# Kernel tuning notes

Measured on AMD Instinct MI355X. Metric: run time of the kernel, lower is better.

## Reference

```python
import jax, jax.numpy as jnp
import numpy as np

N_NODES = 50000
N_EDGES = 400000
N_GRAPHS = 500
N_FEAT = 4
EMB = 200
HID = 128


def setup_inputs() -> dict:
    key = jax.random.key(0)
    ks = jax.random.split(key, 16)
    x = jax.random.normal(ks[0], (N_NODES, N_FEAT), dtype=jnp.float32)
    edge_index = jax.random.randint(ks[1], (2, N_EDGES), 0, N_NODES, dtype=jnp.int64)
    x_scalar = jax.random.normal(ks[2], (N_GRAPHS, N_FEAT), dtype=jnp.float32)
    batch_index = jnp.sort(jax.random.randint(ks[3], (N_NODES,), 0, N_GRAPHS, dtype=jnp.int64))

    def lin(k, fan_in, fan_out):
        return jax.random.normal(k, (fan_in, fan_out), dtype=jnp.float32) / np.sqrt(fan_in)

    params = {
        'W0': lin(ks[4], N_FEAT, EMB), 'b0': jnp.zeros((EMB,), jnp.float32),
        'W1': lin(ks[5], EMB, EMB), 'b1': jnp.zeros((EMB,), jnp.float32),
        'W2': lin(ks[6], EMB, EMB), 'b2': jnp.zeros((EMB,), jnp.float32),
        'W3': lin(ks[7], EMB, EMB), 'b3': jnp.zeros((EMB,), jnp.float32),
        'Wl1': lin(ks[8], EMB + N_FEAT, HID),
        'bl1': jax.random.normal(ks[9], (HID,), jnp.float32) * 0.01,
        'Wl2': lin(ks[10], HID, 1),
        'bl2': jax.random.normal(ks[11], (1,), jnp.float32) * 0.01,
    }
    return dict(x=x, edge_index=edge_index, x_scalar=x_scalar, batch_index=batch_index, **params)


def _gcn_conv(h, W, b, src, dst, norm, num_nodes):
    # PyG GCNConv: h' = D^-1/2 (A+I) D^-1/2 (h W) + b, with precomputed edge norms
    m = (h @ W)[src] * norm[:, None]            # [E+N, out]
    out = jax.ops.segment_sum(m, dst, num_segments=num_nodes)
    return out + b


def reference(x, edge_index, x_scalar, batch_index,
              W0, b0, W1, b1, W2, b2, W3, b3, Wl1, bl1, Wl2, bl2):
    num_nodes = x.shape[0]
    loops = jnp.arange(num_nodes, dtype=edge_index.dtype)
    src = jnp.concatenate([edge_index[0], loops])  # self-loops appended
    dst = jnp.concatenate([edge_index[1], loops])
    deg = jax.ops.segment_sum(jnp.ones_like(dst, dtype=x.dtype), dst, num_segments=num_nodes)
    dinv = deg ** -0.5                              # deg >= 1 due to self-loops
    norm = dinv[src] * dinv[dst]

    h = jax.nn.leaky_relu(_gcn_conv(x, W0, b0, src, dst, norm, num_nodes), 0.01)
    h = jax.nn.leaky_relu(_gcn_conv(h, W1, b1, src, dst, norm, num_nodes), 0.01)
    h = jax.nn.leaky_relu(_gcn_conv(h, W2, b2, src, dst, norm, num_nodes), 0.01)
    h = jax.nn.leaky_relu(_gcn_conv(h, W3, b3, src, dst, norm, num_nodes), 0.01)

    # global mean pool per graph
    sums = jax.ops.segment_sum(h, batch_index, num_segments=N_GRAPHS)
    cnt = jax.ops.segment_sum(jnp.ones((num_nodes,), h.dtype), batch_index, num_segments=N_GRAPHS)
    pooled = sums / jnp.maximum(cnt, 1.0)[:, None]

    g = jnp.concatenate([pooled, x_scalar], axis=1)   # [G, EMB+4]
    g = jax.nn.leaky_relu(g @ Wl1 + bl1, 0.01)
    out = g @ Wl2 + bl2                                # [G, 1]
    return out
```

## Files before the change

kernel.cpp:

```cpp
#include <hip/hip_runtime.h>
#include <math.h>

#define LEAKY(v) ((v) > 0.0f ? (v) : 0.01f * (v))

typedef _Float16 v8h __attribute__((ext_vector_type(8)));
typedef float v4f __attribute__((ext_vector_type(4)));

__global__ void k_count(const int* __restrict__ ei, int* __restrict__ cnt, int E) {
    int e = blockIdx.x * blockDim.x + threadIdx.x;
    if (e < E) atomicAdd(&cnt[ei[E + e]], 1);
}

__global__ __launch_bounds__(256) void k_scan1(const int* __restrict__ cnt,
                                               int* __restrict__ rowptr,
                                               int* __restrict__ bsum, int n) {
    __shared__ int s[256];
    int t = threadIdx.x, i = blockIdx.x * 256 + t;
    int v = (i < n) ? cnt[i] : 0;
    s[t] = v;
    __syncthreads();
    for (int off = 1; off < 256; off <<= 1) {
        int u = (t >= off) ? s[t - off] : 0;
        __syncthreads();
        s[t] += u;
        __syncthreads();
    }
    if (i < n) rowptr[i] = s[t] - v;
    if (t == 255) bsum[blockIdx.x] = s[255];
}

__global__ __launch_bounds__(256) void k_scan3(int* __restrict__ rowptr,
                                               const int* __restrict__ bsum,
                                               const int* __restrict__ cnt,
                                               float* __restrict__ dinv, int n) {
    __shared__ int sred[256];
    int t = threadIdx.x;
    int accum = 0;
    for (int b = t; b < (int)blockIdx.x; b += 256) accum += bsum[b];
    sred[t] = accum;
    __syncthreads();
    for (int off = 128; off > 0; off >>= 1) {
        if (t < off) sred[t] += sred[t + off];
        __syncthreads();
    }
    int base = sred[0];
    int i = blockIdx.x * 256 + t;
    if (i < n) {
        rowptr[i] += base;
        dinv[i] = rsqrtf(1.0f + (float)cnt[i]);
    }
}

__global__ void k_fill(const int* __restrict__ ei, const float* __restrict__ dinv,
                       int* __restrict__ rowptr, int2* __restrict__ adj, int E) {
    int e = blockIdx.x * blockDim.x + threadIdx.x;
    if (e < E) {
        int s = ei[e], d = ei[E + e];
        int pos = atomicAdd(&rowptr[d], 1);
        adj[pos] = make_int2(s, __float_as_int(dinv[s] * dinv[d]));
    }
}

__global__ __launch_bounds__(256) void k_splitW3(const float* __restrict__ W1,
                                                 const float* __restrict__ W2,
                                                 const float* __restrict__ W3,
                                                 _Float16* __restrict__ th0, _Float16* __restrict__ tl0,
                                                 _Float16* __restrict__ th1, _Float16* __restrict__ tl1,
                                                 _Float16* __restrict__ th2, _Float16* __restrict__ tl2,
                                                 int* __restrict__ cnt, int n) {
    int layer = blockIdx.y;
    const float* W = (layer == 0) ? W1 : (layer == 1) ? W2 : W3;
    _Float16* Wth = (layer == 0) ? th0 : (layer == 1) ? th1 : th2;
    _Float16* Wtl = (layer == 0) ? tl0 : (layer == 1) ? tl1 : tl2;
    int idx = blockIdx.x * blockDim.x + threadIdx.x;
    int gidx = (blockIdx.y * gridDim.x + blockIdx.x) * 256 + threadIdx.x;
    for (int j = gidx; j < n; j += gridDim.x * gridDim.y * 256) cnt[j] = 0;
    if (idx >= 224 * 208) return;
    int k = idx / 208, c = idx - k * 208;
    float v = (k < 200 && c < 200) ? W[k * 200 + c] : 0.0f;
    _Float16 hi = (_Float16)v;
    _Float16 lo = (_Float16)(v - (float)hi);
    Wth[c * 224 + k] = hi;
    Wtl[c * 224 + k] = lo;
}

__global__ __launch_bounds__(512, 4) void k_gemm200_mfma_l0(const float* __restrict__ x,
                                                            const float* __restrict__ dinv,
                                                            const int* __restrict__ rowptr,
                                                            const int2* __restrict__ adj,
                                                            const float* __restrict__ W0,
                                                            const float* __restrict__ b0,
                                                            const _Float16* __restrict__ Wth,
                                                            const _Float16* __restrict__ Wtl,
                                                            _Float16* __restrict__ T, int M) {
    __shared__ _Float16 Wsh[2][208 * 32];
    __shared__ _Float16 Wsl[2][208 * 32];
    __shared__ float W0s[4][200];
    __shared__ float b0s[200];
    const int tid  = threadIdx.x;
    const int lane = tid & 63;
    const int wid  = tid >> 6;
    const int quad = lane >> 4;
    const int l16  = lane & 15;
    const int rowA = blockIdx.x * 128 + wid * 16 + l16;
    const int rowAc = min(rowA, M - 1);

    const int nr0 = tid >> 2, p0 = tid & 3;
    const bool two = (tid < 320);
    const int nr1 = nr0 + 128;
    uint4 rh0, rl0, rh1, rl1;
    rh0 = *(const uint4*)&Wth[nr0 * 224 + p0 * 8];
    rl0 = *(const uint4*)&Wtl[nr0 * 224 + p0 * 8];
    if (two) {
        rh1 = *(const uint4*)&Wth[nr1 * 224 + p0 * 8];
        rl1 = *(const uint4*)&Wtl[nr1 * 224 + p0 * 8];
    }

    for (int idx = tid; idx < 1000; idx += 512) {
        if (idx < 800) W0s[idx / 200][idx % 200] = W0[idx];
        else b0s[idx - 800] = b0[idx - 800];
    }

    float w0n = dinv[rowAc]; w0n *= w0n;
    float4 xv = ((const float4*)x)[rowAc];
    float4 pxv = make_float4(xv.x * w0n, xv.y * w0n, xv.z * w0n, xv.w * w0n);
    {
        int lo = rowAc ? rowptr[rowAc - 1] : 0;
        int hi = rowptr[rowAc];
        for (int j = lo; j < hi; ++j) {
            int2 cw = adj[j];
            float w = __int_as_float(cw.y);
            float4 sv = ((const float4*)x)[cw.x];
            pxv.x += sv.x * w; pxv.y += sv.y * w; pxv.z += sv.z * w; pxv.w += sv.w * w;
        }
    }

    v4f acc[13];
#pragma unroll
    for (int t = 0; t < 13; ++t) acc[t] = 0.0f;

#pragma unroll
    for (int kc = 0; kc < 7; ++kc) {
        const int k0 = kc * 32;
        const int buf = kc & 1;
        *(uint4*)&Wsh[buf][nr0 * 32 + p0 * 8] = rh0;
        *(uint4*)&Wsl[buf][nr0 * 32 + p0 * 8] = rl0;
        if (two) {
            *(uint4*)&Wsh[buf][nr1 * 32 + p0 * 8] = rh1;
            *(uint4*)&Wsl[buf][nr1 * 32 + p0 * 8] = rl1;
        }
        if (kc < 6) {
            rh0 = *(const uint4*)&Wth[nr0 * 224 + (k0 + 32) + p0 * 8];
            rl0 = *(const uint4*)&Wtl[nr0 * 224 + (k0 + 32) + p0 * 8];
            if (two) {
                rh1 = *(const uint4*)&Wth[nr1 * 224 + (k0 + 32) + p0 * 8];
                rl1 = *(const uint4*)&Wtl[nr1 * 224 + (k0 + 32) + p0 * 8];
            }
        }
        __syncthreads();
        v8h ah, al;
        int kb = k0 + quad * 8;
        if (kb < 200) {
#pragma unroll
            for (int j = 0; j < 8; ++j) {
                int k = kb + j;
                float pv = pxv.x * W0s[0][k] + pxv.y * W0s[1][k]
                         + pxv.z * W0s[2][k] + pxv.w * W0s[3][k] + b0s[k];
                pv = LEAKY(pv);
                _Float16 h = (_Float16)pv;
                ah[j] = h;
                al[j] = (_Float16)(pv - (float)h);
            }
        } else {
#pragma unroll
            for (int j = 0; j < 8; ++j) { ah[j] = (_Float16)0.0f; al[j] = (_Float16)0.0f; }
        }
#pragma unroll
        for (int t = 0; t < 13; ++t) {
            int nidx = (t * 16 + l16) * 32 + quad * 8;
            v8h wh = *(const v8h*)&Wsh[buf][nidx];
            v8h wl = *(const v8h*)&Wsl[buf][nidx];
            acc[t] = __builtin_amdgcn_mfma_f32_16x16x32_f16(ah, wh, acc[t], 0, 0, 0);
            acc[t] = __builtin_amdgcn_mfma_f32_16x16x32_f16(ah, wl, acc[t], 0, 0, 0);
            acc[t] = __builtin_amdgcn_mfma_f32_16x16x32_f16(al, wh, acc[t], 0, 0, 0);
        }
    }
    const int rb = blockIdx.x * 128 + wid * 16 + quad * 4;
#pragma unroll
    for (int t = 0; t < 13; ++t) {
        int c = t * 16 + l16;
        if (c < 200) {
#pragma unroll
            for (int e = 0; e < 4; ++e) {
                int r = rb + e;
                if (r < M) T[(size_t)r * 200 + c] = (_Float16)acc[t][e];
            }
        }
    }
}

__global__ __launch_bounds__(512, 4) void k_gemm200_mfma(const _Float16* __restrict__ P,
                                                         const float* __restrict__ bias,
                                                         const _Float16* __restrict__ Wth,
                                                         const _Float16* __restrict__ Wtl,
                                                         _Float16* __restrict__ T, int M) {
    __shared__ _Float16 Wsh[2][208 * 32];
    __shared__ _Float16 Wsl[2][208 * 32];
    __shared__ float bS[200];
    const int tid  = threadIdx.x;
    const int lane = tid & 63;
    const int wid  = tid >> 6;
    const int quad = lane >> 4;
    const int l16  = lane & 15;
    const int rowA = blockIdx.x * 128 + wid * 16 + l16;
    const int rowAc = min(rowA, M - 1);
    const _Float16* Prow = P + (size_t)rowAc * 200;

    const int nr0 = tid >> 2, p0 = tid & 3;
    const bool two = (tid < 320);
    const int nr1 = nr0 + 128;
    uint4 rh0, rl0, rh1, rl1;
    rh0 = *(const uint4*)&Wth[nr0 * 224 + p0 * 8];
    rl0 = *(const uint4*)&Wtl[nr0 * 224 + p0 * 8];
    if (two) {
        rh1 = *(const uint4*)&Wth[nr1 * 224 + p0 * 8];
        rl1 = *(const uint4*)&Wtl[nr1 * 224 + p0 * 8];
    }
    if (tid < 200) bS[tid] = bias[tid];

    v8h pch[7];
#pragma unroll
    for (int kc = 0; kc < 7; ++kc) {
        int kb = kc * 32 + quad * 8;
        if (kb < 200) {
            pch[kc] = *(const v8h*)(Prow + kb);
        } else {
#pragma unroll
            for (int j = 0; j < 8; ++j) pch[kc][j] = (_Float16)0.0f;
        }
    }

    v4f acc[13];
#pragma unroll
    for (int t = 0; t < 13; ++t) acc[t] = 0.0f;

#pragma unroll
    for (int kc = 0; kc < 7; ++kc) {
        const int k0 = kc * 32;
        const int buf = kc & 1;
        *(uint4*)&Wsh[buf][nr0 * 32 + p0 * 8] = rh0;
        *(uint4*)&Wsl[buf][nr0 * 32 + p0 * 8] = rl0;
        if (two) {
            *(uint4*)&Wsh[buf][nr1 * 32 + p0 * 8] = rh1;
            *(uint4*)&Wsl[buf][nr1 * 32 + p0 * 8] = rl1;
        }
        if (kc < 6) {
            rh0 = *(const uint4*)&Wth[nr0 * 224 + (k0 + 32) + p0 * 8];
            rl0 = *(const uint4*)&Wtl[nr0 * 224 + (k0 + 32) + p0 * 8];
            if (two) {
                rh1 = *(const uint4*)&Wth[nr1 * 224 + (k0 + 32) + p0 * 8];
                rl1 = *(const uint4*)&Wtl[nr1 * 224 + (k0 + 32) + p0 * 8];
            }
        }
        __syncthreads();
        v8h ah, al;
        int kb = k0 + quad * 8;
        if (kb < 200) {
            v8h ph = pch[kc];
#pragma unroll
            for (int j = 0; j < 8; ++j) {
                float av = (float)ph[j] + bS[kb + j];
                av = LEAKY(av);
                _Float16 h = (_Float16)av;
                ah[j] = h;
                al[j] = (_Float16)(av - (float)h);
            }
        } else {
#pragma unroll
            for (int j = 0; j < 8; ++j) { ah[j] = (_Float16)0.0f; al[j] = (_Float16)0.0f; }
        }
#pragma unroll
        for (int t = 0; t < 13; ++t) {
            int nidx = (t * 16 + l16) * 32 + quad * 8;
            v8h wh = *(const v8h*)&Wsh[buf][nidx];
            v8h wl = *(const v8h*)&Wsl[buf][nidx];
            acc[t] = __builtin_amdgcn_mfma_f32_16x16x32_f16(ah, wh, acc[t], 0, 0, 0);
            acc[t] = __builtin_amdgcn_mfma_f32_16x16x32_f16(ah, wl, acc[t], 0, 0, 0);
            acc[t] = __builtin_amdgcn_mfma_f32_16x16x32_f16(al, wh, acc[t], 0, 0, 0);
        }
    }
    const int rb = blockIdx.x * 128 + wid * 16 + quad * 4;
#pragma unroll
    for (int t = 0; t < 13; ++t) {
        int c = t * 16 + l16;
        if (c < 200) {
#pragma unroll
            for (int e = 0; e < 4; ++e) {
                int r = rb + e;
                if (r < M) T[(size_t)r * 200 + c] = (_Float16)acc[t][e];
            }
        }
    }
}

__global__ __launch_bounds__(256) void k_gather200h(const _Float16* __restrict__ t,
                                                    const float* __restrict__ dinv,
                                                    const int* __restrict__ rowptr,
                                                    const int2* __restrict__ adj,
                                                    _Float16* __restrict__ p, int n) {
    int gid = blockIdx.x * blockDim.x + threadIdx.x;
    if (gid >= n * 25) return;
    int v = gid / 25, c8 = gid - v * 25;
    const v8h* tp = (const v8h*)t;
    float w0 = dinv[v]; w0 *= w0;
    v8h tv = tp[v * 25 + c8];
    float a0[8], a1[8], a2[8], a3[8];
#pragma unroll
    for (int i = 0; i < 8; ++i) { a0[i] = (float)tv[i] * w0; a1[i] = 0.0f; a2[i] = 0.0f; a3[i] = 0.0f; }
    int lo = v ? rowptr[v - 1] : 0;
    int hi = rowptr[v];
    int j = lo;
    for (; j + 3 < hi; j += 4) {
        int2 e0 = adj[j], e1 = adj[j + 1], e2 = adj[j + 2], e3 = adj[j + 3];
        float wa = __int_as_float(e0.y), wb = __int_as_float(e1.y);
        float wc = __int_as_float(e2.y), wd = __int_as_float(e3.y);
        v8h s0 = tp[e0.x * 25 + c8];
        v8h s1 = tp[e1.x * 25 + c8];
        v8h s2 = tp[e2.x * 25 + c8];
        v8h s3 = tp[e3.x * 25 + c8];
#pragma unroll
        for (int i = 0; i < 8; ++i) {
            a0[i] += (float)s0[i] * wa;
            a1[i] += (float)s1[i] * wb;
            a2[i] += (float)s2[i] * wc;
            a3[i] += (float)s3[i] * wd;
        }
    }
    for (; j < hi; ++j) {
        int2 cw = adj[j];
        float w = __int_as_float(cw.y);
        v8h sv = tp[cw.x * 25 + c8];
#pragma unroll
        for (int i = 0; i < 8; ++i) a0[i] += (float)sv[i] * w;
    }
    v8h o;
#pragma unroll
    for (int i = 0; i < 8; ++i) o[i] = (_Float16)((a0[i] + a1[i]) + (a2[i] + a3[i]));
    ((v8h*)p)[v * 25 + c8] = o;
}

__global__ __launch_bounds__(256) void k_poolhead(const _Float16* __restrict__ T,
                                                  const float* __restrict__ b3,
                                                  const int* __restrict__ batch, int n,
                                                  const float* __restrict__ xs,
                                                  const float* __restrict__ Wl1,
                                                  const float* __restrict__ bl1,
                                                  const float* __restrict__ Wl2,
                                                  const float* __restrict__ bl2,
                                                  float* __restrict__ out) {
    __shared__ float part[10][25][9];
    __shared__ float grow[204];
    __shared__ float partial[2];
    __shared__ int sb[2];
    int g = blockIdx.x;
    int t = threadIdx.x;
    if (t == 0 || t == 64) {
        int target = g + (t ? 1 : 0);
        int lo = 0, hi = n;
        while (lo < hi) { int m = (lo + hi) >> 1; if (batch[m] < target) lo = m + 1; else hi = m; }
        sb[t ? 1 : 0] = lo;
    }
    __syncthreads();
    int lo = sb[0], hi = sb[1];
    int c8 = t % 25, li = t / 25;
    if (li < 10) {
        const v8h* tp = (const v8h*)T;
        float4 ba = *(const float4*)(b3 + c8 * 8);
        float4 bb = *(const float4*)(b3 + c8 * 8 + 4);
        float bv[8] = {ba.x, ba.y, ba.z, ba.w, bb.x, bb.y, bb.z, bb.w};
        float acc[8];
#pragma unroll
        for (int i = 0; i < 8; ++i) acc[i] = 0.0f;
        for (int i = lo + li; i < hi; i += 10) {
            v8h tv = tp[(size_t)i * 25 + c8];
#pragma unroll
            for (int jj = 0; jj < 8; ++jj) {
                float v = (float)tv[jj] + bv[jj];
                acc[jj] += LEAKY(v);
            }
        }
#pragma unroll
        for (int jj = 0; jj < 8; ++jj) part[li][c8][jj] = acc[jj];
    }
    __syncthreads();
    if (t < 200) {
        float s = 0.0f;
#pragma unroll
        for (int l2 = 0; l2 < 10; ++l2) s += part[l2][t >> 3][t & 7];
        grow[t] = s / fmaxf((float)(hi - lo), 1.0f);
    } else if (t < 204) {
        grow[t] = xs[g * 4 + (t - 200)];
    }
    __syncthreads();
    if (t < 128) {
        float s = bl1[t];
        for (int k = 0; k < 204; ++k) s += grow[k] * Wl1[k * 128 + t];
        s = LEAKY(s);
        float hv = s * Wl2[t];
        for (int off = 32; off > 0; off >>= 1) hv += __shfl_down(hv, off, 64);
        if ((t & 63) == 0) partial[t >> 6] = hv;
    }
    __syncthreads();
    if (t == 0) out[g] = partial[0] + partial[1] + bl2[0];
}

extern "C" void kernel_launch(void* const* d_in, const int* in_sizes, int n_in,
                              void* d_out, int out_size, void* d_ws, size_t ws_size,
                              hipStream_t stream) {
    const float* x    = (const float*)d_in[0];
    const int*   ei   = (const int*)d_in[1];
    const float* xs   = (const float*)d_in[2];
    const int*   batch= (const int*)d_in[3];
    const float* W0   = (const float*)d_in[4];
    const float* b0   = (const float*)d_in[5];
    const float* W1   = (const float*)d_in[6];
    const float* b1   = (const float*)d_in[7];
    const float* W2   = (const float*)d_in[8];
    const float* b2   = (const float*)d_in[9];
    const float* W3   = (const float*)d_in[10];
    const float* b3   = (const float*)d_in[11];
    const float* Wl1  = (const float*)d_in[12];
    const float* bl1  = (const float*)d_in[13];
    const float* Wl2  = (const float*)d_in[14];
    const float* bl2  = (const float*)d_in[15];
    float* out = (float*)d_out;

    const int N = in_sizes[0] / 4;
    const int E = in_sizes[1] / 2;
    const int G = in_sizes[2] / 4;

    char* ws = (char*)d_ws;
    size_t off = 0;
    auto alloc = [&](size_t bytes) { void* p = ws + off; off += (bytes + 255) & ~size_t(255); return p; };
    _Float16* bufA = (_Float16*)alloc((size_t)N * 200 * sizeof(_Float16));
    _Float16* bufB = (_Float16*)alloc((size_t)N * 200 * sizeof(_Float16));
    float* dinv   = (float*)alloc((size_t)N * sizeof(float));
    int*   cnt    = (int*)alloc((size_t)N * sizeof(int));
    int*   rowptr = (int*)alloc(((size_t)N + 1) * sizeof(int));
    int*   bsum   = (int*)alloc(256 * sizeof(int));
    int2*  adj    = (int2*)alloc((size_t)E * sizeof(int2));
    _Float16* Wth[3]; _Float16* Wtl[3];
    for (int i = 0; i < 3; ++i) {
        Wth[i] = (_Float16*)alloc(208 * 224 * sizeof(_Float16));
        Wtl[i] = (_Float16*)alloc(208 * 224 * sizeof(_Float16));
    }

    const int B = 256;
    const int nblk = (N + 255) / 256;

    dim3 sg((224 * 208 + B - 1) / B, 3);
    k_splitW3<<<sg, B, 0, stream>>>(W1, W2, W3, Wth[0], Wtl[0], Wth[1], Wtl[1], Wth[2], Wtl[2],
                                    cnt, N);

    k_count<<<(E + B - 1) / B, B, 0, stream>>>(ei, cnt, E);
    k_scan1<<<nblk, 256, 0, stream>>>(cnt, rowptr, bsum, N);
    k_scan3<<<nblk, 256, 0, stream>>>(rowptr, bsum, cnt, dinv, N);
    k_fill<<<(E + B - 1) / B, B, 0, stream>>>(ei, dinv, rowptr, adj, E);

    const int gblocks = (N * 25 + 255) / 256;
    const int mblocks = (N + 127) / 128;

    k_gemm200_mfma_l0<<<mblocks, 512, 0, stream>>>(x, dinv, rowptr, adj, W0, b0,
                                                   Wth[0], Wtl[0], bufA, N);
    k_gather200h<<<gblocks, 256, 0, stream>>>(bufA, dinv, rowptr, adj, bufB, N);

    k_gemm200_mfma<<<mblocks, 512, 0, stream>>>(bufB, b1, Wth[1], Wtl[1], bufA, N);
    k_gather200h<<<gblocks, 256, 0, stream>>>(bufA, dinv, rowptr, adj, bufB, N);
    k_gemm200_mfma<<<mblocks, 512, 0, stream>>>(bufB, b2, Wth[2], Wtl[2], bufA, N);
    k_gather200h<<<gblocks, 256, 0, stream>>>(bufA, dinv, rowptr, adj, bufB, N);

    k_poolhead<<<G, 256, 0, stream>>>(bufB, b3, batch, N, xs, Wl1, bl1, Wl2, bl2, out);
}
```

Before: 331.6 us.

## Fuse CSR-build prologue kernels into one cooperative kernel with grid syncs

Replaces the five prologue launches (weight split, degree count, two scan passes, adjacency fill) with a single cooperative kernel of 512 blocks that uses grid.sync between phases. The block-sum scan is now done redundantly in shared memory per chunk instead of a per-block loop over prior sums. This removes launch overhead and inter-kernel gaps. In exchange, each phase runs on a fixed grid with grid-stride loops, and the grid barriers carry their own cost. The second scan also assumes at most 256 chunks, which holds for N=50000.

Result: slower. 578.4 us (+74.4%).

```diff
diff --git a/kernel.cpp b/kernel.cpp
--- a/kernel.cpp
+++ b/kernel.cpp
@@ -1,87 +1,89 @@
 #include <hip/hip_runtime.h>
+#include <hip/hip_cooperative_groups.h>
 #include <math.h>
+
+namespace cg = cooperative_groups;
 
 #define LEAKY(v) ((v) > 0.0f ? (v) : 0.01f * (v))
 
 typedef _Float16 v8h __attribute__((ext_vector_type(8)));
 typedef float v4f __attribute__((ext_vector_type(4)));
 
-__global__ void k_count(const int* __restrict__ ei, int* __restrict__ cnt, int E) {
-    int e = blockIdx.x * blockDim.x + threadIdx.x;
-    if (e < E) atomicAdd(&cnt[ei[E + e]], 1);
-}
-
-__global__ __launch_bounds__(256) void k_scan1(const int* __restrict__ cnt,
-                                               int* __restrict__ rowptr,
-                                               int* __restrict__ bsum, int n) {
+__global__ __launch_bounds__(256) void k_prol(
+    const float* __restrict__ W1, const float* __restrict__ W2, const float* __restrict__ W3,
+    _Float16* __restrict__ th0, _Float16* __restrict__ tl0,
+    _Float16* __restrict__ th1, _Float16* __restrict__ tl1,
+    _Float16* __restrict__ th2, _Float16* __restrict__ tl2,
+    const int* __restrict__ ei, int* __restrict__ cnt, int* __restrict__ rowptr,
+    int* __restrict__ bsum, float* __restrict__ dinv, int2* __restrict__ adj,
+    int N, int E) {
+    cg::grid_group grid = cg::this_grid();
     __shared__ int s[256];
-    int t = threadIdx.x, i = blockIdx.x * 256 + t;
-    int v = (i < n) ? cnt[i] : 0;
-    s[t] = v;
-    __syncthreads();
-    for (int off = 1; off < 256; off <<= 1) {
-        int u = (t >= off) ? s[t - off] : 0;
-        __syncthreads();
-        s[t] += u;
-        __syncthreads();
-    }
-    if (i < n) rowptr[i] = s[t] - v;
-    if (t == 255) bsum[blockIdx.x] = s[255];
-}
-
-__global__ __launch_bounds__(256) void k_scan3(int* __restrict__ rowptr,
-                                               const int* __restrict__ bsum,
-                                               const int* __restrict__ cnt,
-                                               float* __restrict__ dinv, int n) {
-    __shared__ int sred[256];
-    int t = threadIdx.x;
-    int accum = 0;
-    for (int b = t; b < (int)blockIdx.x; b += 256) accum += bsum[b];
-    sred[t] = accum;
-    __syncthreads();
-    for (int off = 128; off > 0; off >>= 1) {
-        if (t < off) sred[t] += sred[t + off];
-        __syncthreads();
-    }
-    int base = sred[0];
-    int i = blockIdx.x * 256 + t;
-    if (i < n) {
-        rowptr[i] += base;
-        dinv[i] = rsqrtf(1.0f + (float)cnt[i]);
-    }
-}
-
-__global__ void k_fill(const int* __restrict__ ei, const float* __restrict__ dinv,
-                       int* __restrict__ rowptr, int2* __restrict__ adj, int E) {
-    int e = blockIdx.x * blockDim.x + threadIdx.x;
-    if (e < E) {
-        int s = ei[e], d = ei[E + e];
+    const int t = threadIdx.x;
+    const int gtid = blockIdx.x * 256 + t;
+    const int gsz = gridDim.x * 256;
+
+    for (int i = gtid; i < N; i += gsz) cnt[i] = 0;
+    for (int idx = gtid; idx < 224 * 208 * 3; idx += gsz) {
+        int layer = idx / (224 * 208);
+        int r = idx - layer * (224 * 208);
+        int k = r / 208, c = r - k * 208;
+        const float* W = (layer == 0) ? W1 : (layer == 1) ? W2 : W3;
+        _Float16* Th = (layer == 0) ? th0 : (layer == 1) ? th1 : th2;
+        _Float16* Tl = (layer == 0) ? tl0 : (layer == 1) ? tl1 : tl2;
+        float v = (k < 200 && c < 200) ? W[k * 200 + c] : 0.0f;
+        _Float16 hi = (_Float16)v;
+        Th[c * 224 + k] = hi;
+        Tl[c * 224 + k] = (_Float16)(v - (float)hi);
+    }
+    grid.sync();
+
+    for (int e = gtid; e < E; e += gsz) atomicAdd(&cnt[ei[E + e]], 1);
+    grid.sync();
+
+    const int nchunk = (N + 255) / 256;
+    for (int c = blockIdx.x; c < nchunk; c += gridDim.x) {
+        int i = c * 256 + t;
+        int v = (i < N) ? cnt[i] : 0;
+        s[t] = v;
+        __syncthreads();
+        for (int off = 1; off < 256; off <<= 1) {
+            int u = (t >= off) ? s[t - off] : 0;
+            __syncthreads();
+            s[t] += u;
+            __syncthreads();
+        }
+        if (i < N) rowptr[i] = s[t] - v;
+        if (t == 255) bsum[c] = s[255];
+        __syncthreads();
+    }
+    grid.sync();
+
+    for (int c = blockIdx.x; c < nchunk; c += gridDim.x) {
+        int v = (t < nchunk) ? bsum[t] : 0;
+        s[t] = v;
+        __syncthreads();
+        for (int off = 1; off < 256; off <<= 1) {
+            int u = (t >= off) ? s[t - off] : 0;
+            __syncthreads();
+            s[t] += u;
+            __syncthreads();
+        }
+        int base = c ? s[c - 1] : 0;
+        int i = c * 256 + t;
+        if (i < N) {
+            rowptr[i] += base;
+            dinv[i] = rsqrtf(1.0f + (float)cnt[i]);
+        }
+        __syncthreads();
+    }
+    grid.sync();
+
+    for (int e = gtid; e < E; e += gsz) {
+        int sv = ei[e], d = ei[E + e];
         int pos = atomicAdd(&rowptr[d], 1);
-        adj[pos] = make_int2(s, __float_as_int(dinv[s] * dinv[d]));
-    }
-}
-
-__global__ __launch_bounds__(256) void k_splitW3(const float* __restrict__ W1,
-                                                 const float* __restrict__ W2,
-                                                 const float* __restrict__ W3,
-                                                 _Float16* __restrict__ th0, _Float16* __restrict__ tl0,
-                                                 _Float16* __restrict__ th1, _Float16* __restrict__ tl1,
-                                                 _Float16* __restrict__ th2, _Float16* __restrict__ tl2,
-                                                 int* __restrict__ cnt, int n) {
-    int layer = blockIdx.y;
-    const float* W = (layer == 0) ? W1 : (layer == 1) ? W2 : W3;
-    _Float16* Wth = (layer == 0) ? th0 : (layer == 1) ? th1 : th2;
-    _Float16* Wtl = (layer == 0) ? tl0 : (layer == 1) ? tl1 : tl2;
-    int idx = blockIdx.x * blockDim.x + threadIdx.x;
-    int gidx = (blockIdx.y * gridDim.x + blockIdx.x) * 256 + threadIdx.x;
-    for (int j = gidx; j < n; j += gridDim.x * gridDim.y * 256) cnt[j] = 0;
-    if (idx >= 224 * 208) return;
-    int k = idx / 208, c = idx - k * 208;
-    float v = (k < 200 && c < 200) ? W[k * 200 + c] : 0.0f;
-    _Float16 hi = (_Float16)v;
-    _Float16 lo = (_Float16)(v - (float)hi);
-    Wth[c * 224 + k] = hi;
-    Wtl[c * 224 + k] = lo;
+        adj[pos] = make_int2(sv, __float_as_int(dinv[sv] * dinv[d]));
+    }
 }
 
 __global__ __launch_bounds__(512, 4) void k_gemm200_mfma_l0(const float* __restrict__ x,
@@ -455,17 +457,18 @@
         Wtl[i] = (_Float16*)alloc(208 * 224 * sizeof(_Float16));
     }
 
-    const int B = 256;
-    const int nblk = (N + 255) / 256;
-
-    dim3 sg((224 * 208 + B - 1) / B, 3);
-    k_splitW3<<<sg, B, 0, stream>>>(W1, W2, W3, Wth[0], Wtl[0], Wth[1], Wtl[1], Wth[2], Wtl[2],
-                                    cnt, N);
-
-    k_count<<<(E + B - 1) / B, B, 0, stream>>>(ei, cnt, E);
-    k_scan1<<<nblk, 256, 0, stream>>>(cnt, rowptr, bsum, N);
-    k_scan3<<<nblk, 256, 0, stream>>>(rowptr, bsum, cnt, dinv, N);
-    k_fill<<<(E + B - 1) / B, B, 0, stream>>>(ei, dinv, rowptr, adj, E);
+    {
+        int Nv = N, Ev = E;
+        const float *a0 = W1, *a1 = W2, *a2 = W3;
+        _Float16 *p0 = Wth[0], *p1 = Wtl[0], *p2 = Wth[1], *p3 = Wtl[1], *p4 = Wth[2], *p5 = Wtl[2];
+        const int* pei = ei;
+        int *pcnt = cnt, *prow = rowptr, *pbsum = bsum;
+        float* pdinv = dinv;
+        int2* padj = adj;
+        void* args[] = {&a0, &a1, &a2, &p0, &p1, &p2, &p3, &p4, &p5,
+                        &pei, &pcnt, &prow, &pbsum, &pdinv, &padj, &Nv, &Ev};
+        hipLaunchCooperativeKernel((void*)k_prol, dim3(512), dim3(256), args, 0, stream);
+    }
 
     const int gblocks = (N * 25 + 255) / 256;
     const int mblocks = (N + 127) / 128;
```

## Fuse final GCN gather with mean pooling via per-segment atomics

Applied to the files above, without the earlier changes.

The last neighbour aggregation is folded into the pooling stage. Each 32-node chunk gathers neighbour rows, adds bias, applies leaky ReLU and accumulates per-graph sums, which are added into a zeroed pooled buffer with atomics. A small head kernel then finishes the MLP. This removes the write and re-read of a full N x 200 half-precision buffer and the poolhead pass, which had only 500 blocks and so used the GPU poorly. In exchange it adds float atomics, with order-dependent summation, and a zeroing step placed in k_scan3.

Result: no change. 328.3 us, median of 3 (-1.0%).

```diff
diff --git a/kernel.cpp b/kernel.cpp
--- a/kernel.cpp
+++ b/kernel.cpp
@@ -32,7 +32,8 @@
 __global__ __launch_bounds__(256) void k_scan3(int* __restrict__ rowptr,
                                                const int* __restrict__ bsum,
                                                const int* __restrict__ cnt,
-                                               float* __restrict__ dinv, int n) {
+                                               float* __restrict__ dinv, int n,
+                                               float* __restrict__ pooled, int npool) {
     __shared__ int sred[256];
     int t = threadIdx.x;
     int accum = 0;
@@ -49,6 +50,7 @@
         rowptr[i] += base;
         dinv[i] = rsqrtf(1.0f + (float)cnt[i]);
     }
+    for (int j = i; j < npool; j += gridDim.x * 256) pooled[j] = 0.0f;
 }
 
 __global__ void k_fill(const int* __restrict__ ei, const float* __restrict__ dinv,
@@ -349,16 +351,90 @@
     ((v8h*)p)[v * 25 + c8] = o;
 }
 
-__global__ __launch_bounds__(256) void k_poolhead(const _Float16* __restrict__ T,
-                                                  const float* __restrict__ b3,
-                                                  const int* __restrict__ batch, int n,
-                                                  const float* __restrict__ xs,
-                                                  const float* __restrict__ Wl1,
-                                                  const float* __restrict__ bl1,
-                                                  const float* __restrict__ Wl2,
-                                                  const float* __restrict__ bl2,
-                                                  float* __restrict__ out) {
+__global__ __launch_bounds__(256) void k_gpool(const _Float16* __restrict__ T,
+                                               const float* __restrict__ dinv,
+                                               const int* __restrict__ rowptr,
+                                               const int2* __restrict__ adj,
+                                               const float* __restrict__ b3,
+                                               const int* __restrict__ batch, int n,
+                                               float* __restrict__ pooled) {
     __shared__ float part[10][25][9];
+    const int t = threadIdx.x;
+    const int c8 = t % 25, li = t / 25;
+    const int base = blockIdx.x * 32;
+    const int end = min(base + 32, n);
+    const v8h* tp = (const v8h*)T;
+    float4 ba = *(const float4*)(b3 + c8 * 8);
+    float4 bb = *(const float4*)(b3 + c8 * 8 + 4);
+    float bv[8] = {ba.x, ba.y, ba.z, ba.w, bb.x, bb.y, bb.z, bb.w};
+
+    int seg = base;
+    while (seg < end) {
+        int g = batch[seg];
+        int lo2 = seg + 1, hi2 = end;
+        while (lo2 < hi2) { int m = (lo2 + hi2) >> 1; if (batch[m] == g) lo2 = m + 1; else hi2 = m; }
+        int segend = lo2;
+
+        if (li < 10) {
+            float acc[8];
+#pragma unroll
+            for (int i = 0; i < 8; ++i) acc[i] = 0.0f;
+            for (int i = seg + li; i < segend; i += 10) {
+                float w0 = dinv[i]; w0 *= w0;
+                v8h tv = tp[(size_t)i * 25 + c8];
+                float a0[8], a1[8];
+#pragma unroll
+                for (int q = 0; q < 8; ++q) { a0[q] = (float)tv[q] * w0; a1[q] = 0.0f; }
+                int elo = i ? rowptr[i - 1] : 0;
+                int ehi = rowptr[i];
+                int j = elo;
+                for (; j + 1 < ehi; j += 2) {
+                    int2 e0 = adj[j], e1 = adj[j + 1];
+                    float wa = __int_as_float(e0.y), wb = __int_as_float(e1.y);
+                    v8h s0 = tp[(size_t)e0.x * 25 + c8];
+                    v8h s1 = tp[(size_t)e1.x * 25 + c8];
+#pragma unroll
+                    for (int q = 0; q < 8; ++q) {
+                        a0[q] += (float)s0[q] * wa;
+                        a1[q] += (float)s1[q] * wb;
+                    }
+                }
+                if (j < ehi) {
+                    int2 cw = adj[j];
+                    float w = __int_as_float(cw.y);
+                    v8h sv = tp[(size_t)cw.x * 25 + c8];
+#pragma unroll
+                    for (int q = 0; q < 8; ++q) a0[q] += (float)sv[q] * w;
+                }
+#pragma unroll
+                for (int q = 0; q < 8; ++q) {
+                    float v = a0[q] + a1[q] + bv[q];
+                    acc[q] += LEAKY(v);
+                }
+            }
+#pragma unroll
+            for (int q = 0; q < 8; ++q) part[li][c8][q] = acc[q];
+        }
+        __syncthreads();
+        if (t < 200) {
+            float s = 0.0f;
+#pragma unroll
+            for (int l2 = 0; l2 < 10; ++l2) s += part[l2][t >> 3][t & 7];
+            atomicAdd(&pooled[g * 200 + t], s);
+        }
+        __syncthreads();
+        seg = segend;
+    }
+}
+
+__global__ __launch_bounds__(128) void k_headfin(const float* __restrict__ pooled,
+                                                 const int* __restrict__ batch, int n_nodes,
+                                                 const float* __restrict__ xs,
+                                                 const float* __restrict__ Wl1,
+                                                 const float* __restrict__ bl1,
+                                                 const float* __restrict__ Wl2,
+                                                 const float* __restrict__ bl2,
+                                                 float* __restrict__ out) {
     __shared__ float grow[204];
     __shared__ float partial[2];
     __shared__ int sb[2];
@@ -366,50 +442,21 @@
     int t = threadIdx.x;
     if (t == 0 || t == 64) {
         int target = g + (t ? 1 : 0);
-        int lo = 0, hi = n;
+        int lo = 0, hi = n_nodes;
         while (lo < hi) { int m = (lo + hi) >> 1; if (batch[m] < target) lo = m + 1; else hi = m; }
         sb[t ? 1 : 0] = lo;
     }
     __syncthreads();
-    int lo = sb[0], hi = sb[1];
-    int c8 = t % 25, li = t / 25;
-    if (li < 10) {
-        const v8h* tp = (const v8h*)T;
-        float4 ba = *(const float4*)(b3 + c8 * 8);
-        float4 bb = *(const float4*)(b3 + c8 * 8 + 4);
-        float bv[8] = {ba.x, ba.y, ba.z, ba.w, bb.x, bb.y, bb.z, bb.w};
-        float acc[8];
-#pragma unroll
-        for (int i = 0; i < 8; ++i) acc[i] = 0.0f;
-        for (int i = lo + li; i < hi; i += 10) {
-            v8h tv = tp[(size_t)i * 25 + c8];
-#pragma unroll
-            for (int jj = 0; jj < 8; ++jj) {
-                float v = (float)tv[jj] + bv[jj];
-                acc[jj] += LEAKY(v);
-            }
-        }
-#pragma unroll
-        for (int jj = 0; jj < 8; ++jj) part[li][c8][jj] = acc[jj];
-    }
+    float inv = 1.0f / fmaxf((float)(sb[1] - sb[0]), 1.0f);
+    for (int idx = t; idx < 200; idx += 128) grow[idx] = pooled[g * 200 + idx] * inv;
+    if (t < 4) grow[200 + t] = xs[g * 4 + t];
     __syncthreads();
-    if (t < 200) {
-        float s = 0.0f;
-#pragma unroll
-        for (int l2 = 0; l2 < 10; ++l2) s += part[l2][t >> 3][t & 7];
-        grow[t] = s / fmaxf((float)(hi - lo), 1.0f);
-    } else if (t < 204) {
-        grow[t] = xs[g * 4 + (t - 200)];
-    }
-    __syncthreads();
-    if (t < 128) {
-        float s = bl1[t];
-        for (int k = 0; k < 204; ++k) s += grow[k] * Wl1[k * 128 + t];
-        s = LEAKY(s);
-        float hv = s * Wl2[t];
-        for (int off = 32; off > 0; off >>= 1) hv += __shfl_down(hv, off, 64);
-        if ((t & 63) == 0) partial[t >> 6] = hv;
-    }
+    float s = bl1[t];
+    for (int k = 0; k < 204; ++k) s += grow[k] * Wl1[k * 128 + t];
+    s = LEAKY(s);
+    float hv = s * Wl2[t];
+    for (int off = 32; off > 0; off >>= 1) hv += __shfl_down(hv, off, 64);
+    if ((t & 63) == 0) partial[t >> 6] = hv;
     __syncthreads();
     if (t == 0) out[g] = partial[0] + partial[1] + bl2[0];
 }
@@ -445,6 +492,7 @@
     _Float16* bufA = (_Float16*)alloc((size_t)N * 200 * sizeof(_Float16));
     _Float16* bufB = (_Float16*)alloc((size_t)N * 200 * sizeof(_Float16));
     float* dinv   = (float*)alloc((size_t)N * sizeof(float));
+    float* pooled = (float*)alloc((size_t)G * 200 * sizeof(float));
     int*   cnt    = (int*)alloc((size_t)N * sizeof(int));
     int*   rowptr = (int*)alloc(((size_t)N + 1) * sizeof(int));
     int*   bsum   = (int*)alloc(256 * sizeof(int));
@@ -464,7 +512,7 @@
 
     k_count<<<(E + B - 1) / B, B, 0, stream>>>(ei, cnt, E);
     k_scan1<<<nblk, 256, 0, stream>>>(cnt, rowptr, bsum, N);
-    k_scan3<<<nblk, 256, 0, stream>>>(rowptr, bsum, cnt, dinv, N);
+    k_scan3<<<nblk, 256, 0, stream>>>(rowptr, bsum, cnt, dinv, N, pooled, G * 200);
     k_fill<<<(E + B - 1) / B, B, 0, stream>>>(ei, dinv, rowptr, adj, E);
 
     const int gblocks = (N * 25 + 255) / 256;
@@ -477,7 +525,7 @@
     k_gemm200_mfma<<<mblocks, 512, 0, stream>>>(bufB, b1, Wth[1], Wtl[1], bufA, N);
     k_gather200h<<<gblocks, 256, 0, stream>>>(bufA, dinv, rowptr, adj, bufB, N);
     k_gemm200_mfma<<<mblocks, 512, 0, stream>>>(bufB, b2, Wth[2], Wtl[2], bufA, N);
-    k_gather200h<<<gblocks, 256, 0, stream>>>(bufA, dinv, rowptr, adj, bufB, N);
-
-    k_poolhead<<<G, 256, 0, stream>>>(bufB, b3, batch, N, xs, Wl1, bl1, Wl2, bl2, out);
-}
+
+    k_gpool<<<(N + 31) / 32, 256, 0, stream>>>(bufA, dinv, rowptr, adj, b3, batch, N, pooled);
+    k_headfin<<<G, 128, 0, stream>>>(pooled, batch, N, xs, Wl1, bl1, Wl2, bl2, out);
+}
```
